# Kernel optimization log

Hardware: AMD Instinct MI355X
Metric: run time of the kernel (lower is better)

The kernel has to match this reference:

```python
import jax, jax.numpy as jnp
import numpy as np

B = 4096


def setup_inputs() -> dict:
    key = jax.random.key(0)
    u = jax.random.uniform(key, (B, 5), dtype=jnp.float32)
    centers = u[:, :2] * 64.0          # box centers in [0, 64)
    wh = u[:, 2:4] * 8.0 + 1.0         # widths/heights in [1, 9)
    ang = u[:, 4:5] * 3.14159265       # rotation angle in [0, pi)
    boxes = jnp.concatenate([centers, wh, ang], axis=-1)  # (B,5)
    return {"boxes": boxes}


def _rect_to_corners(boxes):
    # boxes: (B,5) = (x, y, w, h, theta) -> corners (B,4,2)
    unit = jnp.array([[-1.0, -1.0], [1.0, -1.0], [1.0, 1.0], [-1.0, 1.0]],
                     dtype=boxes.dtype)
    ctr, wh, ang = boxes[:, :2], boxes[:, 2:4], boxes[:, 4]
    base = unit[None, :, :] * (wh * 0.5)[:, None, :]        # (B,4,2)
    c, s = jnp.cos(ang), jnp.sin(ang)
    rot = jnp.stack([jnp.stack([c, -s], -1),
                     jnp.stack([s, c], -1)], axis=1)         # (B,2,2)
    return jnp.einsum('bkd,bde->bke', base, rot) + ctr[:, None, :]


def _giou1d(min1, max1, min2, max2):
    # exact (non-fast) 1-D GIoU per axis
    inter = jnp.clip(jnp.minimum(max1, max2) - jnp.maximum(min1, min2), 0.0)
    union = (max1 - min1) + (max2 - min2) - inter
    hull = jnp.maximum(max1, max2) - jnp.minimum(min1, min2)
    return inter / union - (hull - union) / hull


def reference(boxes):
    corners = _rect_to_corners(boxes)                        # (B,4,2)
    nb = corners.shape[0]
    # two edge axes per box: c1-c0 and c3-c0
    axes = jnp.stack([corners[:, 1] - corners[:, 0],
                      corners[:, 3] - corners[:, 0]], axis=1)  # (B,2,2)
    # self projections: box b's corners onto its own axes
    sp = jnp.einsum('bkd,bad->bak', corners, axes)           # (B,2,4)
    smin, smax = sp.min(-1), sp.max(-1)                      # (B,2)
    # cross projections: corners of box i onto axes of box j
    cp = jnp.einsum('ikd,jad->ijak', corners, axes)          # (B,B,2,4)
    cmin, cmax = cp.min(-1), cp.max(-1)                      # (B,B,2)
    # projections of box j's corners onto box i's axes = transpose of cross
    cminT, cmaxT = jnp.swapaxes(cmin, 0, 1), jnp.swapaxes(cmax, 0, 1)
    # axes of box i: (box i self) vs (box j projected on i's axes)
    gA = _giou1d(smin[:, None, :], smax[:, None, :], cminT, cmaxT)  # (B,B,2)
    # axes of box j: (box i projected on j's axes) vs (box j self)
    gB = _giou1d(cmin, cmax, smin[None, :, :], smax[None, :, :])    # (B,B,2)
    g = jnp.concatenate([gA, gB], axis=-1).min(-1)           # min over 4 axes
    pairwise = jnp.clip(g, 0.0)
    idx = jnp.arange(nb)
    pairwise = pairwise.at[idx, idx].set(0.0)                # zero diagonal
    return pairwise  # reduction='none' -> (B,B)
```

## Files before the change

### kernel.cpp

```cpp
#include <hip/hip_runtime.h>
#include <math.h>

#define NBOX 4096
#define TILE 32
#define NT (NBOX / TILE)
#define NBLK (NT * (NT + 1) / 2)
#define SS 12
#define JB 400

typedef float v2f __attribute__((ext_vector_type(2)));
typedef float vf4 __attribute__((ext_vector_type(4)));


struct Box {
    v2f A0, A1, SC, LL;
    float cx, cy;
};

__device__ __forceinline__ float rcp_fast(float x) { return __builtin_amdgcn_rcpf(x); }
__device__ __forceinline__ v2f splat(float s) { return (v2f){s, s}; }
__device__ __forceinline__ v2f fma2(v2f a, v2f b, v2f c) { return __builtin_elementwise_fma(a, b, c); }
__device__ __forceinline__ v2f abs2(v2f a) { return __builtin_elementwise_abs(a); }

__device__ __forceinline__ float mgiou_pair(const Box& I, const Box& J) {
    v2f dA = fma2(I.A0, splat(J.A0.x), I.A1 * J.A1.x);
    v2f dB = fma2(I.A0, splat(J.A0.y), I.A1 * J.A1.y);
    v2f DI = fma2(I.A0, splat(J.cx), fma2(I.A1, splat(J.cy), -I.SC));
    v2f DJ = fma2(J.A0, splat(I.cx), fma2(J.A1, splat(I.cy), -J.SC));
    v2f aA = abs2(dA), aB = abs2(dB);
    v2f HI = aA + aB;
    float HJ0 = aA.x + aA.y;
    float HJ1 = aB.x + aB.y;
    v2f SI = I.LL + HI;
    float SJ0 = J.LL.x + HJ0, SJ1 = J.LL.y + HJ1;
    v2f uI = fma2(splat(0.5f), SI, -abs2(DI));
    float uJ0 = fmaf(0.5f, SJ0, -fabsf(DJ.x));
    float uJ1 = fmaf(0.5f, SJ1, -fabsf(DJ.y));
    float r0 = fminf(fminf(I.LL.x, HI.x), uI.x);
    float r1 = fminf(fminf(I.LL.y, HI.y), uI.y);
    float r2 = fminf(fminf(J.LL.x, HJ0), uJ0);
    float r3 = fminf(fminf(J.LL.y, HJ1), uJ1);
    float g0 = r0 * rcp_fast(SI.x - r0);
    float g1 = r1 * rcp_fast(SI.y - r1);
    float g2 = r2 * rcp_fast(SJ0 - r2);
    float g3 = r3 * rcp_fast(SJ1 - r3);
    float g = fminf(fminf(g0, g1), fminf(g2, g3));
    return fmaxf(g, 0.0f);
}

__device__ __forceinline__ int sw_offset(int i) { return i * SS + (i >> 3) * 4; }

__device__ __forceinline__ Box load_box(const float* p) {
    Box b;
    float4 x = *(const float4*)(p);
    float4 y = *(const float4*)(p + 4);
    float2 z = *(const float2*)(p + 8);
    b.A0 = (v2f){x.x, x.y}; b.A1 = (v2f){x.z, x.w};
    b.SC = (v2f){y.x, y.y}; b.LL = (v2f){y.z, y.w};
    b.cx = z.x; b.cy = z.y;
    return b;
}

__global__ __launch_bounds__(64)
void pairwise_kernel(const float* __restrict__ boxes, float* __restrict__ out) {
    int k = blockIdx.x;
    int bi = (int)((float)(2 * NT + 1 - sqrtf((float)((2 * NT + 1) * (2 * NT + 1) - 8 * k))) * 0.5f);
    if (bi > 0 && k < bi * NT - bi * (bi - 1) / 2) bi--;
    if (k >= (bi + 1) * NT - (bi + 1) * bi / 2) bi++;
    int bj = bi + (k - (bi * NT - bi * (bi - 1) / 2));

    __shared__ float sm[JB + 400];

    int tid = threadIdx.x;
    {
        int loc = tid & (TILE - 1);
        int box = ((tid < TILE) ? bi : bj) * TILE + loc;
        float cx = boxes[box * 5 + 0];
        float cy = boxes[box * 5 + 1];
        float w  = boxes[box * 5 + 2];
        float h  = boxes[box * 5 + 3];
        float ang = boxes[box * 5 + 4];
        float s, c;
        __sincosf(ang, &s, &c);
        float a0x = w * c, a0y = -w * s;
        float a1x = h * s, a1y =  h * c;
        float sc0 = fmaf(a0x, cx, a0y * cy);
        float sc1 = fmaf(a1x, cx, a1y * cy);
        float* d = &sm[((tid < TILE) ? 0 : JB) + sw_offset(loc)];
        ((float4*)d)[0] = make_float4(a0x, a1x, a0y, a1y);
        ((float4*)d)[1] = make_float4(sc0, sc1, w * w, h * h);
        ((float2*)d)[4] = make_float2(cx, cy);
    }
    __syncthreads();

    int tx = tid & 7;
    int ty = tid >> 3;
    Box J[4];
    const float* jp = &sm[JB + sw_offset(4 * tx)];
    #pragma unroll
    for (int m = 0; m < 4; ++m) J[m] = load_box(jp + m * SS);

    int ibase = bi * TILE, jbase = bj * TILE;
    bool offdiag = (bi != bj);
    const float* ip = &sm[sw_offset(4 * ty)];
    float vT[4][4];

    #pragma unroll
    for (int kk = 0; kk < 4; ++kk) {
        Box I = load_box(ip + kk * SS);
        int ig = ibase + 4 * ty + kk;
        float v[4];
        #pragma unroll
        for (int m = 0; m < 4; ++m) {
            int jg = jbase + 4 * tx + m;
            v[m] = (ig == jg) ? 0.0f : mgiou_pair(I, J[m]);
            vT[m][kk] = v[m];
        }
        vf4 o = {v[0], v[1], v[2], v[3]};
        __builtin_nontemporal_store(o, (vf4*)&out[(size_t)ig * NBOX + jbase + 4 * tx]);
    }

    if (offdiag) {
        #pragma unroll
        for (int m = 0; m < 4; ++m) {
            int jg = jbase + 4 * tx + m;
            vf4 o = {vT[m][0], vT[m][1], vT[m][2], vT[m][3]};
            __builtin_nontemporal_store(o, (vf4*)&out[(size_t)jg * NBOX + ibase + 4 * ty]);
        }
    }
}

extern "C" void kernel_launch(void* const* d_in, const int* in_sizes, int n_in,
                              void* d_out, int out_size, void* d_ws, size_t ws_size,
                              hipStream_t stream) {
    const float* boxes = (const float*)d_in[0];
    float* out = (float*)d_out;
    pairwise_kernel<<<dim3(NBLK), dim3(64), 0, stream>>>(boxes, out);
}
```

Measured before the change: 81.02 us.

## Pack four triangle tiles per 512-thread block and fuse the GIoU reciprocals into one

Each block now handles four upper-triangle 32x32 tiles with 512 threads, two wavefronts per tile, and each thread computes a 4x2 patch instead of 4x4. The pair function is rewritten to cross-multiply the four ratios so only a single reciprocal is needed, and the min/abs work is vectorized into v2f ops. Stores switch from nontemporal to regular, and forward rows are written as 8-byte stores. The aim is to cut per-block launch overhead and the per-pair transcendental cost, in exchange for narrower stores and a possible change in rounding or overflow behaviour from the product-based division.

```diff
diff --git a/kernel.cpp b/kernel.cpp
--- a/kernel.cpp
+++ b/kernel.cpp
@@ -4,9 +4,11 @@
 #define NBOX 4096
 #define TILE 32
 #define NT (NBOX / TILE)
-#define NBLK (NT * (NT + 1) / 2)
+#define NTRI (NT * (NT + 1) / 2)
+#define NBLK (NTRI / 4)
 #define SS 12
 #define JB 400
+#define SLICE 800
 
 typedef float v2f __attribute__((ext_vector_type(2)));
 typedef float vf4 __attribute__((ext_vector_type(4)));
@@ -21,6 +23,7 @@
 __device__ __forceinline__ v2f splat(float s) { return (v2f){s, s}; }
 __device__ __forceinline__ v2f fma2(v2f a, v2f b, v2f c) { return __builtin_elementwise_fma(a, b, c); }
 __device__ __forceinline__ v2f abs2(v2f a) { return __builtin_elementwise_abs(a); }
+__device__ __forceinline__ v2f min2(v2f a, v2f b) { return __builtin_elementwise_min(a, b); }
 
 __device__ __forceinline__ float mgiou_pair(const Box& I, const Box& J) {
     v2f dA = fma2(I.A0, splat(J.A0.x), I.A1 * J.A1.x);
@@ -29,23 +32,19 @@
     v2f DJ = fma2(J.A0, splat(I.cx), fma2(J.A1, splat(I.cy), -J.SC));
     v2f aA = abs2(dA), aB = abs2(dB);
     v2f HI = aA + aB;
-    float HJ0 = aA.x + aA.y;
-    float HJ1 = aB.x + aB.y;
+    v2f HJ = (v2f){aA.x, aB.x} + (v2f){aA.y, aB.y};
     v2f SI = I.LL + HI;
-    float SJ0 = J.LL.x + HJ0, SJ1 = J.LL.y + HJ1;
+    v2f SJ = J.LL + HJ;
     v2f uI = fma2(splat(0.5f), SI, -abs2(DI));
-    float uJ0 = fmaf(0.5f, SJ0, -fabsf(DJ.x));
-    float uJ1 = fmaf(0.5f, SJ1, -fabsf(DJ.y));
-    float r0 = fminf(fminf(I.LL.x, HI.x), uI.x);
-    float r1 = fminf(fminf(I.LL.y, HI.y), uI.y);
-    float r2 = fminf(fminf(J.LL.x, HJ0), uJ0);
-    float r3 = fminf(fminf(J.LL.y, HJ1), uJ1);
-    float g0 = r0 * rcp_fast(SI.x - r0);
-    float g1 = r1 * rcp_fast(SI.y - r1);
-    float g2 = r2 * rcp_fast(SJ0 - r2);
-    float g3 = r3 * rcp_fast(SJ1 - r3);
-    float g = fminf(fminf(g0, g1), fminf(g2, g3));
-    return fmaxf(g, 0.0f);
+    v2f uJ = fma2(splat(0.5f), SJ, -abs2(DJ));
+    v2f rI = min2(min2(I.LL, HI), uI);
+    v2f rJ = min2(min2(J.LL, HJ), uJ);
+    float S01 = SI.x * SI.y, S23 = SJ.x * SJ.y;
+    float P = S01 * S23;
+    v2f mI = rI * (v2f){SI.y, SI.x} * splat(S23);
+    v2f mJ = rJ * (v2f){SJ.y, SJ.x} * splat(S01);
+    float mm = fminf(fminf(mI.x, mI.y), fminf(mJ.x, mJ.y));
+    return fmaxf(mm, 0.0f) * rcp_fast(P - mm);
 }
 
 __device__ __forceinline__ int sw_offset(int i) { return i * SS + (i >> 3) * 4; }
@@ -61,20 +60,23 @@
     return b;
 }
 
-__global__ __launch_bounds__(64)
-void pairwise_kernel(const float* __restrict__ boxes, float* __restrict__ out) {
-    int k = blockIdx.x;
-    int bi = (int)((float)(2 * NT + 1 - sqrtf((float)((2 * NT + 1) * (2 * NT + 1) - 8 * k))) * 0.5f);
+__device__ __forceinline__ void decode_tri(int k, int& bi, int& bj) {
+    bi = (int)((float)(2 * NT + 1 - sqrtf((float)((2 * NT + 1) * (2 * NT + 1) - 8 * k))) * 0.5f);
     if (bi > 0 && k < bi * NT - bi * (bi - 1) / 2) bi--;
     if (k >= (bi + 1) * NT - (bi + 1) * bi / 2) bi++;
-    int bj = bi + (k - (bi * NT - bi * (bi - 1) / 2));
+    bj = bi + (k - (bi * NT - bi * (bi - 1) / 2));
+}
 
-    __shared__ float sm[JB + 400];
+__global__ __launch_bounds__(512, 8)
+void pairwise_kernel(const float* __restrict__ boxes, float* __restrict__ out) {
+    __shared__ float sm[4 * SLICE];
 
     int tid = threadIdx.x;
-    {
-        int loc = tid & (TILE - 1);
-        int box = ((tid < TILE) ? bi : bj) * TILE + loc;
+    if (tid < 256) {
+        int sid = tid >> 6, loc = tid & 63;
+        int kP = 4 * blockIdx.x + sid;
+        int biP, bjP; decode_tri(kP, biP, bjP);
+        int box = ((loc < TILE) ? biP : bjP) * TILE + (loc & (TILE - 1));
         float cx = boxes[box * 5 + 0];
         float cy = boxes[box * 5 + 1];
         float w  = boxes[box * 5 + 2];
@@ -86,46 +88,50 @@
         float a1x = h * s, a1y =  h * c;
         float sc0 = fmaf(a0x, cx, a0y * cy);
         float sc1 = fmaf(a1x, cx, a1y * cy);
-        float* d = &sm[((tid < TILE) ? 0 : JB) + sw_offset(loc)];
+        float* d = &sm[sid * SLICE + ((loc < TILE) ? 0 : JB) + sw_offset(loc & (TILE - 1))];
         ((float4*)d)[0] = make_float4(a0x, a1x, a0y, a1y);
         ((float4*)d)[1] = make_float4(sc0, sc1, w * w, h * h);
         ((float2*)d)[4] = make_float2(cx, cy);
     }
     __syncthreads();
 
-    int tx = tid & 7;
-    int ty = tid >> 3;
-    Box J[4];
-    const float* jp = &sm[JB + sw_offset(4 * tx)];
-    #pragma unroll
-    for (int m = 0; m < 4; ++m) J[m] = load_box(jp + m * SS);
+    int w8 = tid >> 6;
+    int s = w8 >> 1;
+    int hf = w8 & 1;
+    int lane = tid & 63;
+    int jq = lane & 15;
+    int tg = lane >> 4;
+    int rbase = 16 * hf + 4 * tg;
+
+    int k = 4 * blockIdx.x + s;
+    int bi, bj; decode_tri(k, bi, bj);
+
+    const float* base = &sm[s * SLICE];
+    Box J0 = load_box(base + JB + sw_offset(2 * jq));
+    Box J1 = load_box(base + JB + sw_offset(2 * jq + 1));
 
     int ibase = bi * TILE, jbase = bj * TILE;
-    bool offdiag = (bi != bj);
-    const float* ip = &sm[sw_offset(4 * ty)];
-    float vT[4][4];
+    const float* ip = base + sw_offset(rbase);
+    float vT[2][4];
 
     #pragma unroll
     for (int kk = 0; kk < 4; ++kk) {
         Box I = load_box(ip + kk * SS);
-        int ig = ibase + 4 * ty + kk;
-        float v[4];
-        #pragma unroll
-        for (int m = 0; m < 4; ++m) {
-            int jg = jbase + 4 * tx + m;
-            v[m] = (ig == jg) ? 0.0f : mgiou_pair(I, J[m]);
-            vT[m][kk] = v[m];
-        }
-        vf4 o = {v[0], v[1], v[2], v[3]};
-        __builtin_nontemporal_store(o, (vf4*)&out[(size_t)ig * NBOX + jbase + 4 * tx]);
+        int ig = ibase + rbase + kk;
+        int jg0 = jbase + 2 * jq;
+        float v0 = (ig == jg0)     ? 0.0f : mgiou_pair(I, J0);
+        float v1 = (ig == jg0 + 1) ? 0.0f : mgiou_pair(I, J1);
+        vT[0][kk] = v0; vT[1][kk] = v1;
+        v2f o = {v0, v1};
+        *(v2f*)&out[(size_t)ig * NBOX + jg0] = o;
     }
 
-    if (offdiag) {
+    if (bi != bj) {
         #pragma unroll
-        for (int m = 0; m < 4; ++m) {
-            int jg = jbase + 4 * tx + m;
+        for (int m = 0; m < 2; ++m) {
+            int jg = jbase + 2 * jq + m;
             vf4 o = {vT[m][0], vT[m][1], vT[m][2], vT[m][3]};
-            __builtin_nontemporal_store(o, (vf4*)&out[(size_t)jg * NBOX + ibase + 4 * ty]);
+            *(vf4*)&out[(size_t)jg * NBOX + ibase + rbase] = o;
         }
     }
 }
@@ -135,5 +141,5 @@
                               hipStream_t stream) {
     const float* boxes = (const float*)d_in[0];
     float* out = (float*)d_out;
-    pairwise_kernel<<<dim3(NBLK), dim3(64), 0, stream>>>(boxes, out);
+    pairwise_kernel<<<dim3(NBLK), dim3(512), 0, stream>>>(boxes, out);
 }
```

New measurement: 105.8 us. 1.31x slower.
